# Kernel optimization log

Measured on AMD Instinct MI355X. Metric: run time of the kernel, lower is better.

Reference implementation:

```python
import jax, jax.numpy as jnp
import numpy as np
import math

EMBED = 1024
HEADS = 16
HEAD_DIM = EMBED // HEADS
B, S = 2, 2048


def setup_inputs() -> dict:
    key = jax.random.key(0)
    ks = jax.random.split(key, 11)
    s = 1.0 / math.sqrt(EMBED)
    return {
        "query": jax.random.normal(ks[0], (B, S, EMBED), jnp.float32),
        "key_": jax.random.normal(ks[1], (B, S, EMBED), jnp.float32),
        "value": jax.random.normal(ks[2], (B, S, EMBED), jnp.float32),
        "Wq": jax.random.normal(ks[3], (EMBED, EMBED), jnp.float32) * s,
        "bq": jax.random.normal(ks[4], (EMBED,), jnp.float32) * s,
        "Wk": jax.random.normal(ks[5], (EMBED, EMBED), jnp.float32) * s,
        "bk": jax.random.normal(ks[6], (EMBED,), jnp.float32) * s,
        "Wv": jax.random.normal(ks[7], (EMBED, EMBED), jnp.float32) * s,
        "bv": jax.random.normal(ks[8], (EMBED,), jnp.float32) * s,
        "Wo": jax.random.normal(ks[9], (EMBED, EMBED), jnp.float32) * s,
        "bo": jax.random.normal(ks[10], (EMBED,), jnp.float32) * s,
    }


def reference(query, key_, value, Wq, bq, Wk, bk, Wv, bv, Wo, bo):
    b, s, e = query.shape
    # projections (torch Linear: x @ W.T + b)
    q = query @ Wq.T + bq
    k = key_ @ Wk.T + bk
    v = value @ Wv.T + bv
    # [B, H, S, hd]
    q = q.reshape(b, s, HEADS, HEAD_DIM).transpose(0, 2, 1, 3)
    k = k.reshape(b, s, HEADS, HEAD_DIM).transpose(0, 2, 1, 3)
    v = v.reshape(b, s, HEADS, HEAD_DIM).transpose(0, 2, 1, 3)
    scores = jnp.einsum("bhqd,bhkd->bhqk", q, k) / math.sqrt(HEAD_DIM)
    attn = jax.nn.softmax(scores, axis=-1)
    out = jnp.einsum("bhqk,bhkd->bhqd", attn, v)
    out = out.transpose(0, 2, 1, 3).reshape(b, s, e)
    return out @ Wo.T + bo
```

## Files before the change

kernel.cpp:

```cpp
#include <hip/hip_runtime.h>
#include <hip/hip_bf16.h>

using bf16_t = __bf16;
using bf16x4 = __attribute__((ext_vector_type(4))) __bf16;
using bf16x8 = __attribute__((ext_vector_type(8))) __bf16;
using f32x4  = __attribute__((ext_vector_type(4))) float;
using u32 = unsigned int;

constexpr int S_ = 2048, E_ = 1024, M_ = 4096;
constexpr size_t MAT_A = (size_t)M_ * E_;
constexpr size_t MAT_W = (size_t)E_ * E_;

__device__ __forceinline__ bf16_t tobf(float f) {
  unsigned u = __builtin_bit_cast(unsigned, f);
  unsigned short r = (unsigned short)((u + 0x7fffu + ((u >> 16) & 1u)) >> 16);
  return __builtin_bit_cast(bf16_t, r);
}
__device__ __forceinline__ u32 packbf2(float a, float b) {
  u32 ua = __builtin_bit_cast(u32, a) + 0x8000u;
  u32 ub = __builtin_bit_cast(u32, b) + 0x8000u;
  return (ua >> 16) | (ub & 0xffff0000u);
}
__device__ __forceinline__ void async_lds16(const bf16_t* g, bf16_t* l) {
  __builtin_amdgcn_global_load_lds(
      (const __attribute__((address_space(1))) unsigned int*)g,
      (__attribute__((address_space(3))) unsigned int*)l, 16, 0, 0);
}

__global__ __launch_bounds__(256) void cvt_all(
    const float* __restrict__ s0, const float* __restrict__ s1,
    const float* __restrict__ s2, const float* __restrict__ s3,
    const float* __restrict__ s4, const float* __restrict__ s5,
    const float* __restrict__ s6,
    bf16_t* __restrict__ d0, bf16_t* __restrict__ d1,
    bf16_t* __restrict__ d2, bf16_t* __restrict__ d3,
    bf16_t* __restrict__ d4, bf16_t* __restrict__ d5,
    bf16_t* __restrict__ d6) {
  size_t i8 = ((size_t)blockIdx.x * 256 + threadIdx.x) * 8;
  const float* s;
  bf16_t* d;
  size_t off;
  if (i8 < 3 * MAT_A) {
    int w = (int)(i8 >> 22);
    off = i8 & (MAT_A - 1);
    s = w == 0 ? s0 : w == 1 ? s1 : s2;
    d = w == 0 ? d0 : w == 1 ? d1 : d2;
  } else {
    size_t j = i8 - 3 * MAT_A;
    int w = (int)(j >> 20);
    off = j & (MAT_W - 1);
    s = w == 0 ? s3 : w == 1 ? s4 : w == 2 ? s5 : s6;
    d = w == 0 ? d3 : w == 1 ? d4 : w == 2 ? d5 : d6;
  }
  float4 a = *(const float4*)(s + off);
  float4 b = *(const float4*)(s + off + 4);
  bf16x8 o;
  o[0] = tobf(a.x); o[1] = tobf(a.y); o[2] = tobf(a.z); o[3] = tobf(a.w);
  o[4] = tobf(b.x); o[5] = tobf(b.y); o[6] = tobf(b.z); o[7] = tobf(b.w);
  *(bf16x8*)(d + off) = o;
}

__global__ __launch_bounds__(256) void gemm_qkv(
    const bf16_t* __restrict__ xq, const bf16_t* __restrict__ xk,
    const bf16_t* __restrict__ xv, const bf16_t* __restrict__ wq,
    const bf16_t* __restrict__ wk, const bf16_t* __restrict__ wv,
    const float* __restrict__ bq, const float* __restrict__ bk,
    const float* __restrict__ bv, bf16_t* __restrict__ outb,
    bf16_t* __restrict__ Vt) {
  constexpr int K = 1024, N = 1024, BK = 64;
  constexpr float SC = 0.18033688011f;
  __shared__ __align__(16) bf16_t smem[18432];
  bf16_t* As = smem;
  bf16_t* Bs = smem + 128 * BK;

  const int which = blockIdx.y >> 3;
  const bf16_t* X = which == 0 ? xq : which == 1 ? xk : xv;
  const bf16_t* W = which == 0 ? wq : which == 1 ? wk : wv;
  const float* bias = which == 0 ? bq : which == 1 ? bk : bv;
  const int row0 = blockIdx.x * 128, col0 = (blockIdx.y & 7) * 128;

  const int tid = threadIdx.x, lane = tid & 63, wave = tid >> 6;
  const int l15 = lane & 15, q = lane >> 4;
  const int wm = (wave & 1) * 64, wn = (wave >> 1) * 64;
  const f32x4 fzero = {0.f, 0.f, 0.f, 0.f};

  f32x4 acc[4][4];
#pragma unroll
  for (int i = 0; i < 4; ++i)
#pragma unroll
    for (int j = 0; j < 4; ++j) acc[i][j] = fzero;

  const int srow = lane >> 3;
  const int schunk = ((lane & 7) ^ srow) * 8;
  const bf16_t* gA = X + (size_t)(row0 + wave * 32 + srow) * K + schunk;
  const bf16_t* gB = W + (size_t)(col0 + wave * 32 + srow) * K + schunk;
  bf16_t* lA = As + wave * 32 * BK;
  bf16_t* lB = Bs + wave * 32 * BK;

  int ck[2];
  ck[0] = ((q) ^ (l15 & 7)) * 8;
  ck[1] = ((4 + q) ^ (l15 & 7)) * 8;

  for (int k0 = 0; k0 < K; k0 += BK) {
    __syncthreads();
#pragma unroll
    for (int p = 0; p < 4; ++p) {
      async_lds16(gA + k0 + (size_t)(p * 8) * K, lA + p * 8 * BK);
      async_lds16(gB + k0 + (size_t)(p * 8) * K, lB + p * 8 * BK);
    }
    __syncthreads();
#pragma unroll
    for (int h = 0; h < 2; ++h) {
      bf16x8 af[4], bw[4];
#pragma unroll
      for (int i = 0; i < 4; ++i)
        af[i] = *(const bf16x8*)(As + (wm + i * 16 + l15) * BK + ck[h]);
#pragma unroll
      for (int j = 0; j < 4; ++j)
        bw[j] = *(const bf16x8*)(Bs + (wn + j * 16 + l15) * BK + ck[h]);
#pragma unroll
      for (int i = 0; i < 4; ++i)
#pragma unroll
        for (int j = 0; j < 4; ++j)
          acc[i][j] = __builtin_amdgcn_mfma_f32_16x16x32_bf16(af[i], bw[j],
                                                              acc[i][j], 0, 0, 0);
    }
  }

  if (which < 2) {
    const float sc = which == 0 ? SC : 1.0f;
    bf16_t* C = outb + (size_t)which * MAT_A;
#pragma unroll
    for (int j = 0; j < 4; ++j) {
      const int col = col0 + wn + j * 16 + l15;
      const float bc = bias[col];
#pragma unroll
      for (int i = 0; i < 4; ++i)
#pragma unroll
        for (int r = 0; r < 4; ++r) {
          const int row = row0 + wm + i * 16 + q * 4 + r;
          C[(size_t)row * N + col] = tobf((acc[i][j][r] + bc) * sc);
        }
    }
  } else {
    __syncthreads();
    bf16_t* Ep = smem + wave * 4608;
#pragma unroll
    for (int j = 0; j < 4; ++j) {
      const float bc = bias[col0 + wn + j * 16 + l15];
      const int nl = j * 16 + l15;
#pragma unroll
      for (int i = 0; i < 4; ++i) {
        uint2 pk;
        pk.x = packbf2(acc[i][j][0] + bc, acc[i][j][1] + bc);
        pk.y = packbf2(acc[i][j][2] + bc, acc[i][j][3] + bc);
        *(uint2*)(Ep + nl * 72 + i * 16 + q * 4) = pk;
      }
    }
    const int head = (col0 + wn) >> 6;
    const int tok0 = row0 + wm;
    const int bb = tok0 >> 11, tokb = tok0 & 2047;
    const int dl = lane >> 3, ml = (lane & 7) * 8;
#pragma unroll
    for (int p = 0; p < 8; ++p) {
      const int d = dl + p * 8;
      bf16x8 v = *(const bf16x8*)(Ep + d * 72 + ml);
      *(bf16x8*)(Vt + ((size_t)((bb * 16 + head) * 64 + d)) * S_ + tokb + ml) = v;
    }
  }
}

__global__ __launch_bounds__(256) void gemm_o(const bf16_t* __restrict__ X,
                                              const bf16_t* __restrict__ W,
                                              const float* __restrict__ bias,
                                              float* __restrict__ C) {
  constexpr int K = 1024, N = 1024, BK = 64;
  __shared__ __align__(16) bf16_t As[64 * BK];
  __shared__ __align__(16) bf16_t Bs[128 * BK];
  const int tid = threadIdx.x, lane = tid & 63, wave = tid >> 6;
  const int l15 = lane & 15, q = lane >> 4;
  const int row0 = blockIdx.x * 64, col0 = blockIdx.y * 128;
  const int wm = (wave & 1) * 32, wn = (wave >> 1) * 64;
  const f32x4 fzero = {0.f, 0.f, 0.f, 0.f};

  f32x4 acc[2][4];
#pragma unroll
  for (int i = 0; i < 2; ++i)
#pragma unroll
    for (int j = 0; j < 4; ++j) acc[i][j] = fzero;

  const int srow = lane >> 3;
  const int schunk = ((lane & 7) ^ srow) * 8;
  const bf16_t* gA = X + (size_t)(row0 + wave * 16 + srow) * K + schunk;
  const bf16_t* gB = W + (size_t)(col0 + wave * 32 + srow) * K + schunk;
  bf16_t* lA = As + wave * 16 * BK;
  bf16_t* lB = Bs + wave * 32 * BK;

  int ck[2];
  ck[0] = ((q) ^ (l15 & 7)) * 8;
  ck[1] = ((4 + q) ^ (l15 & 7)) * 8;

  for (int k0 = 0; k0 < K; k0 += BK) {
    __syncthreads();
    async_lds16(gA + k0, lA);
    async_lds16(gA + k0 + (size_t)8 * K, lA + 8 * BK);
#pragma unroll
    for (int p = 0; p < 4; ++p)
      async_lds16(gB + k0 + (size_t)(p * 8) * K, lB + p * 8 * BK);
    __syncthreads();
#pragma unroll
    for (int h = 0; h < 2; ++h) {
      bf16x8 af[2], bw[4];
#pragma unroll
      for (int i = 0; i < 2; ++i)
        af[i] = *(const bf16x8*)(As + (wm + i * 16 + l15) * BK + ck[h]);
#pragma unroll
      for (int j = 0; j < 4; ++j)
        bw[j] = *(const bf16x8*)(Bs + (wn + j * 16 + l15) * BK + ck[h]);
#pragma unroll
      for (int i = 0; i < 2; ++i)
#pragma unroll
        for (int j = 0; j < 4; ++j)
          acc[i][j] = __builtin_amdgcn_mfma_f32_16x16x32_bf16(af[i], bw[j],
                                                              acc[i][j], 0, 0, 0);
    }
  }

#pragma unroll
  for (int j = 0; j < 4; ++j) {
    const int col = col0 + wn + j * 16 + l15;
    const float bc = bias[col];
#pragma unroll
    for (int i = 0; i < 2; ++i)
#pragma unroll
      for (int r = 0; r < 4; ++r) {
        const int row = row0 + wm + i * 16 + q * 4 + r;
        C[(size_t)row * N + col] = acc[i][j][r] + bc;
      }
  }
}

__global__ __launch_bounds__(256) void attn_mfma(
    const bf16_t* __restrict__ Qm, const bf16_t* __restrict__ Km,
    const bf16_t* __restrict__ Vtg, bf16_t* __restrict__ Om) {
  constexpr int LDP = 72;
  __shared__ __align__(16) bf16_t Ks[2][64 * 64];
  __shared__ __align__(16) bf16_t Vs[2][64 * 64];
  __shared__ __align__(16) bf16_t Ps[4][2][16 * LDP];

  const int tid = threadIdx.x, lane = tid & 63, wave = tid >> 6;
  const int l15 = lane & 15, q = lane >> 4;
  const int bh = blockIdx.x & 31, qb = blockIdx.x >> 5;
  const int b = bh >> 4, h = bh & 15;
  const size_t rowbase = (size_t)b * S_;
  const int hcol = h * 64;
  const int q0 = qb * 128 + wave * 32;

  const int srow = lane >> 3;
  const int schunk = (lane & 7) ^ srow;
  const bf16_t* gK = Km + (rowbase + wave * 16 + srow) * E_ + hcol + schunk * 8;
  const bf16_t* gV = Vtg + ((size_t)bh * 64 + wave * 16 + srow) * S_ + schunk * 8;

  bf16x8 qf[2][2];
#pragma unroll
  for (int qt = 0; qt < 2; ++qt) {
    const bf16_t* qp = Qm + (rowbase + q0 + qt * 16 + l15) * E_ + hcol + q * 8;
    qf[qt][0] = *(const bf16x8*)qp;
    qf[qt][1] = *(const bf16x8*)(qp + 32);
  }

  bf16x8 onesv;
#pragma unroll
  for (int j = 0; j < 8; ++j)
    onesv[j] = __builtin_bit_cast(bf16_t, (unsigned short)0x3F80);

  const f32x4 fzero = {0.f, 0.f, 0.f, 0.f};
  f32x4 oacc[2][4];
#pragma unroll
  for (int qt = 0; qt < 2; ++qt)
#pragma unroll
    for (int mt = 0; mt < 4; ++mt) oacc[qt][mt] = fzero;
  f32x4 lsacc[2] = {fzero, fzero};

  const int rbase = l15 * 64;
  int ck[2];
  ck[0] = ((q) ^ (l15 & 7)) * 8;
  ck[1] = ((4 + q) ^ (l15 & 7)) * 8;
  bf16_t* pw0 = Ps[wave][0] + l15 * LDP;
  bf16_t* pw1 = Ps[wave][1] + l15 * LDP;

  async_lds16(gK, Ks[0] + wave * 1024);
  async_lds16(gK + (size_t)8 * E_, Ks[0] + wave * 1024 + 512);
  async_lds16(gV, Vs[0] + wave * 1024);
  async_lds16(gV + (size_t)8 * S_, Vs[0] + wave * 1024 + 512);

  for (int t = 0; t < 32; ++t) {
    const int pb = t & 1;
    __syncthreads();
    if (t + 1 < 32) {
      const size_t koff = (size_t)((t + 1) * 64) * E_;
      const int voff = (t + 1) * 64;
      bf16_t* dK = Ks[pb ^ 1] + wave * 1024;
      bf16_t* dV = Vs[pb ^ 1] + wave * 1024;
      async_lds16(gK + koff, dK);
      async_lds16(gK + koff + (size_t)8 * E_, dK + 512);
      async_lds16(gV + voff, dV);
      async_lds16(gV + voff + (size_t)8 * S_, dV + 512);
    }
    const bf16_t* Kbuf = Ks[pb];
    const bf16_t* Vbuf = Vs[pb];

#pragma unroll
    for (int nt = 0; nt < 4; ++nt) {
      bf16x8 a0 = *(const bf16x8*)(Kbuf + nt * 1024 + rbase + ck[0]);
      bf16x8 a1 = *(const bf16x8*)(Kbuf + nt * 1024 + rbase + ck[1]);
#pragma unroll
      for (int qt = 0; qt < 2; ++qt) {
        f32x4 st = fzero;
        st = __builtin_amdgcn_mfma_f32_16x16x32_bf16(a0, qf[qt][0], st, 0, 0, 0);
        st = __builtin_amdgcn_mfma_f32_16x16x32_bf16(a1, qf[qt][1], st, 0, 0, 0);
        uint2 pk;
        pk.x = packbf2(__builtin_amdgcn_exp2f(st[0]), __builtin_amdgcn_exp2f(st[1]));
        pk.y = packbf2(__builtin_amdgcn_exp2f(st[2]), __builtin_amdgcn_exp2f(st[3]));
        *(uint2*)((qt ? pw1 : pw0) + nt * 16 + q * 4) = pk;
      }
    }

#pragma unroll
    for (int kk = 0; kk < 2; ++kk) {
      bf16x8 bp0 = *(const bf16x8*)(pw0 + kk * 32 + q * 8);
      bf16x8 bp1 = *(const bf16x8*)(pw1 + kk * 32 + q * 8);
      lsacc[0] = __builtin_amdgcn_mfma_f32_16x16x32_bf16(onesv, bp0, lsacc[0], 0, 0, 0);
      lsacc[1] = __builtin_amdgcn_mfma_f32_16x16x32_bf16(onesv, bp1, lsacc[1], 0, 0, 0);
#pragma unroll
      for (int mt = 0; mt < 4; ++mt) {
        bf16x8 av = *(const bf16x8*)(Vbuf + mt * 1024 + rbase + ck[kk]);
        oacc[0][mt] = __builtin_amdgcn_mfma_f32_16x16x32_bf16(av, bp0,
                                                              oacc[0][mt], 0, 0, 0);
        oacc[1][mt] = __builtin_amdgcn_mfma_f32_16x16x32_bf16(av, bp1,
                                                              oacc[1][mt], 0, 0, 0);
      }
    }
  }

#pragma unroll
  for (int qt = 0; qt < 2; ++qt) {
    const float inv = 1.0f / lsacc[qt][0];
    const size_t orow = (rowbase + q0 + qt * 16 + l15) * E_ + hcol + q * 4;
#pragma unroll
    for (int mt = 0; mt < 4; ++mt) {
      bf16x4 o;
#pragma unroll
      for (int r = 0; r < 4; ++r) o[r] = tobf(oacc[qt][mt][r] * inv);
      *(bf16x4*)(Om + orow + mt * 16) = o;
    }
  }
}

extern "C" void kernel_launch(void* const* d_in, const int* in_sizes, int n_in,
                              void* d_out, int out_size, void* d_ws, size_t ws_size,
                              hipStream_t stream) {
  const float* query = (const float*)d_in[0];
  const float* key_  = (const float*)d_in[1];
  const float* value = (const float*)d_in[2];
  const float* Wq = (const float*)d_in[3];
  const float* bq = (const float*)d_in[4];
  const float* Wk = (const float*)d_in[5];
  const float* bk = (const float*)d_in[6];
  const float* Wv = (const float*)d_in[7];
  const float* bv = (const float*)d_in[8];
  const float* Wo = (const float*)d_in[9];
  const float* bo = (const float*)d_in[10];

  bf16_t* qc  = (bf16_t*)d_ws;
  bf16_t* kc  = qc + MAT_A;
  bf16_t* vc  = kc + MAT_A;
  bf16_t* wqb = vc + MAT_A;
  bf16_t* wkb = wqb + MAT_W;
  bf16_t* wvb = wkb + MAT_W;
  bf16_t* wob = wvb + MAT_W;
  bf16_t* Qb  = wob + MAT_W;
  bf16_t* Kb  = Qb + MAT_A;
  bf16_t* Vt  = Kb + MAT_A;
  bf16_t* AOb = Vt + MAT_A;

  cvt_all<<<8192, 256, 0, stream>>>(query, key_, value, Wq, Wk, Wv, Wo,
                                    qc, kc, vc, wqb, wkb, wvb, wob);
  gemm_qkv<<<dim3(32, 24), 256, 0, stream>>>(qc, kc, vc, wqb, wkb, wvb,
                                             bq, bk, bv, Qb, Vt);
  attn_mfma<<<512, 256, 0, stream>>>(Qb, Kb, Vt, AOb);
  gemm_o<<<dim3(64, 8), 256, 0, stream>>>(AOb, wob, bo, (float*)d_out);
}
```

Before: 221.6 us.

## Software-pipeline attention loop: overlap QK^T/exp of tile t with PV of tile t-1

Restructures the attention inner loop so each iteration computes scores and exp for the current K tile while doing the P·V MFMAs for the previous tile. V gets triple buffering and P double buffering in LDS to support the lag, with a tail step after the loop. The barrier moves to the end of each iteration and a prologue sync is added. The aim is to hide exp/pack latency and LDS round-trips behind independent MFMA work, at the cost of more LDS use, which may reduce occupancy.

```diff
diff --git a/kernel.cpp b/kernel.cpp
--- a/kernel.cpp
+++ b/kernel.cpp
@@ -244,9 +244,9 @@
     const bf16_t* __restrict__ Qm, const bf16_t* __restrict__ Km,
     const bf16_t* __restrict__ Vtg, bf16_t* __restrict__ Om) {
   constexpr int LDP = 72;
-  __shared__ __align__(16) bf16_t Ks[2][64 * 64];
-  __shared__ __align__(16) bf16_t Vs[2][64 * 64];
-  __shared__ __align__(16) bf16_t Ps[4][2][16 * LDP];
+  __shared__ __align__(16) bf16_t Ks[2][4096];
+  __shared__ __align__(16) bf16_t Vs[3][4096];
+  __shared__ __align__(16) bf16_t Ps[4][2][2 * 16 * LDP];
 
   const int tid = threadIdx.x, lane = tid & 63, wave = tid >> 6;
   const int l15 = lane & 15, q = lane >> 4;
@@ -286,50 +286,90 @@
   int ck[2];
   ck[0] = ((q) ^ (l15 & 7)) * 8;
   ck[1] = ((4 + q) ^ (l15 & 7)) * 8;
-  bf16_t* pw0 = Ps[wave][0] + l15 * LDP;
-  bf16_t* pw1 = Ps[wave][1] + l15 * LDP;
-
-  async_lds16(gK, Ks[0] + wave * 1024);
-  async_lds16(gK + (size_t)8 * E_, Ks[0] + wave * 1024 + 512);
-  async_lds16(gV, Vs[0] + wave * 1024);
-  async_lds16(gV + (size_t)8 * S_, Vs[0] + wave * 1024 + 512);
+  const int prow = l15 * LDP;
+
+  {
+    bf16_t* dK = Ks[0] + wave * 1024;
+    bf16_t* dV = Vs[0] + wave * 1024;
+    async_lds16(gK, dK);
+    async_lds16(gK + (size_t)8 * E_, dK + 512);
+    async_lds16(gV, dV);
+    async_lds16(gV + (size_t)8 * S_, dV + 512);
+  }
+  __syncthreads();
+
+  int vprev = 2;
+  int vcur = 0;
+  int vnext = 1;
 
   for (int t = 0; t < 32; ++t) {
     const int pb = t & 1;
-    __syncthreads();
-    if (t + 1 < 32) {
+    if (t < 31) {
       const size_t koff = (size_t)((t + 1) * 64) * E_;
       const int voff = (t + 1) * 64;
       bf16_t* dK = Ks[pb ^ 1] + wave * 1024;
-      bf16_t* dV = Vs[pb ^ 1] + wave * 1024;
+      bf16_t* dV = Vs[vnext] + wave * 1024;
       async_lds16(gK + koff, dK);
       async_lds16(gK + koff + (size_t)8 * E_, dK + 512);
       async_lds16(gV + voff, dV);
       async_lds16(gV + voff + (size_t)8 * S_, dV + 512);
     }
-    const bf16_t* Kbuf = Ks[pb];
-    const bf16_t* Vbuf = Vs[pb];
-
-#pragma unroll
-    for (int nt = 0; nt < 4; ++nt) {
-      bf16x8 a0 = *(const bf16x8*)(Kbuf + nt * 1024 + rbase + ck[0]);
-      bf16x8 a1 = *(const bf16x8*)(Kbuf + nt * 1024 + rbase + ck[1]);
-#pragma unroll
-      for (int qt = 0; qt < 2; ++qt) {
-        f32x4 st = fzero;
-        st = __builtin_amdgcn_mfma_f32_16x16x32_bf16(a0, qf[qt][0], st, 0, 0, 0);
-        st = __builtin_amdgcn_mfma_f32_16x16x32_bf16(a1, qf[qt][1], st, 0, 0, 0);
-        uint2 pk;
-        pk.x = packbf2(__builtin_amdgcn_exp2f(st[0]), __builtin_amdgcn_exp2f(st[1]));
-        pk.y = packbf2(__builtin_amdgcn_exp2f(st[2]), __builtin_amdgcn_exp2f(st[3]));
-        *(uint2*)((qt ? pw1 : pw0) + nt * 16 + q * 4) = pk;
+
+    {
+      const bf16_t* Kbuf = Ks[pb];
+      bf16_t* pc = Ps[wave][pb];
+#pragma unroll
+      for (int nt = 0; nt < 4; ++nt) {
+        bf16x8 a0 = *(const bf16x8*)(Kbuf + nt * 1024 + rbase + ck[0]);
+        bf16x8 a1 = *(const bf16x8*)(Kbuf + nt * 1024 + rbase + ck[1]);
+#pragma unroll
+        for (int qt = 0; qt < 2; ++qt) {
+          f32x4 st = fzero;
+          st = __builtin_amdgcn_mfma_f32_16x16x32_bf16(a0, qf[qt][0], st, 0, 0, 0);
+          st = __builtin_amdgcn_mfma_f32_16x16x32_bf16(a1, qf[qt][1], st, 0, 0, 0);
+          uint2 pk;
+          pk.x = packbf2(__builtin_amdgcn_exp2f(st[0]), __builtin_amdgcn_exp2f(st[1]));
+          pk.y = packbf2(__builtin_amdgcn_exp2f(st[2]), __builtin_amdgcn_exp2f(st[3]));
+          *(uint2*)(pc + qt * 16 * LDP + prow + nt * 16 + q * 4) = pk;
+        }
       }
     }
 
+    if (t >= 1) {
+      const bf16_t* Vbuf = Vs[vprev];
+      const bf16_t* pp = Ps[wave][pb ^ 1];
+#pragma unroll
+      for (int kk = 0; kk < 2; ++kk) {
+        bf16x8 bp0 = *(const bf16x8*)(pp + prow + kk * 32 + q * 8);
+        bf16x8 bp1 = *(const bf16x8*)(pp + 16 * LDP + prow + kk * 32 + q * 8);
+        lsacc[0] = __builtin_amdgcn_mfma_f32_16x16x32_bf16(onesv, bp0, lsacc[0], 0, 0, 0);
+        lsacc[1] = __builtin_amdgcn_mfma_f32_16x16x32_bf16(onesv, bp1, lsacc[1], 0, 0, 0);
+#pragma unroll
+        for (int mt = 0; mt < 4; ++mt) {
+          bf16x8 av = *(const bf16x8*)(Vbuf + mt * 1024 + rbase + ck[kk]);
+          oacc[0][mt] = __builtin_amdgcn_mfma_f32_16x16x32_bf16(av, bp0,
+                                                                oacc[0][mt], 0, 0, 0);
+          oacc[1][mt] = __builtin_amdgcn_mfma_f32_16x16x32_bf16(av, bp1,
+                                                                oacc[1][mt], 0, 0, 0);
+        }
+      }
+    }
+
+    __syncthreads();
+
+    const int tmp = vprev;
+    vprev = vcur;
+    vcur = vnext;
+    vnext = tmp;
+  }
+
+  {
+    const bf16_t* Vbuf = Vs[vprev];
+    const bf16_t* pp = Ps[wave][1];
 #pragma unroll
     for (int kk = 0; kk < 2; ++kk) {
-      bf16x8 bp0 = *(const bf16x8*)(pw0 + kk * 32 + q * 8);
-      bf16x8 bp1 = *(const bf16x8*)(pw1 + kk * 32 + q * 8);
+      bf16x8 bp0 = *(const bf16x8*)(pp + prow + kk * 32 + q * 8);
+      bf16x8 bp1 = *(const bf16x8*)(pp + 16 * LDP + prow + kk * 32 + q * 8);
       lsacc[0] = __builtin_amdgcn_mfma_f32_16x16x32_bf16(onesv, bp0, lsacc[0], 0, 0, 0);
       lsacc[1] = __builtin_amdgcn_mfma_f32_16x16x32_bf16(onesv, bp1, lsacc[1], 0, 0, 0);
 #pragma unroll
```

New measurement: 231.9 us. +4.7%, slower.
